# Kernel tuning notes

Measured on AMD Instinct MI355X. Metric: run time of the kernel, lower is better.

The kernel has to match this reference:

```python
import jax, jax.numpy as jnp
import numpy as np

N = 8192   # nodes per modality
D = 128    # hidden_channels
H = 2      # transformer heads
R = 15     # relations in HeteroConv (use_speaker='no')
E = 16384  # edges per relation
L = 2      # num_layers
# relation src/dst node-type ids: 0=audio, 1=text, 2=visual (dict order: a/v/t past, a/v/t future, a/v/t self, then cross)
SRC = np.array([0, 2, 1, 0, 2, 1, 0, 2, 1, 0, 0, 2, 2, 1, 1])
DST = np.array([0, 2, 1, 0, 2, 1, 0, 2, 1, 2, 1, 0, 1, 0, 2])


def setup_inputs() -> dict:
    key = jax.random.key(0)
    ks = jax.random.split(key, 18)
    f = lambda k, sh: jax.random.normal(k, sh, dtype=jnp.float32) * 0.05
    return {
        "x_audio": jax.random.normal(ks[0], (N, D), jnp.float32),
        "x_text": jax.random.normal(ks[1], (N, D), jnp.float32),
        "x_visual": jax.random.normal(ks[2], (N, D), jnp.float32),
        "edge_index": jax.random.randint(ks[3], (R, 2, E), 0, N, jnp.int32),
        "Wrel": f(ks[4], (L, R, D, D)),
        "brel": f(ks[5], (L, R, D)),
        "Wroot": f(ks[6], (L, R, D, D)),
        "Wq": f(ks[7], (D, H * D)), "bq": f(ks[8], (H * D,)),
        "Wk": f(ks[9], (D, H * D)), "bk": f(ks[10], (H * D,)),
        "Wv": f(ks[11], (D, H * D)), "bv": f(ks[12], (H * D,)),
        "Wskip": f(ks[13], (D, D)), "bskip": f(ks[14], (D,)),
        "gamma": jnp.ones((D,), jnp.float32),
        "beta": jnp.zeros((D,), jnp.float32),
    }


def reference(x_audio, x_text, x_visual, edge_index, Wrel, brel, Wroot,
              Wq, bq, Wk, bk, Wv, bv, Wskip, bskip, gamma, beta):
    src_t = jnp.asarray(SRC)
    dst_t = jnp.asarray(DST)
    x = jnp.stack([x_audio, x_text, x_visual])           # [3, N, D]
    src_idx = edge_index[:, 0]                            # [R, E]
    dst_idx = edge_index[:, 1]                            # [R, E]
    rel = jnp.arange(R)

    # --- HeteroConv of 15 GraphConvs (aggr='add' inside, 'mean' over the 5 relations per dst type) ---
    seg = (rel[:, None] * N + dst_idx).reshape(-1)        # per-relation segment ids
    for l in range(L):
        feats = jnp.take_along_axis(x[src_t], src_idx[:, :, None], axis=1)     # [R, E, D]
        msg = jax.ops.segment_sum(feats.reshape(R * E, D), seg,
                                  num_segments=R * N).reshape(R, N, D)          # scatter-add per relation
        out = (jnp.einsum('rnd,rde->rne', msg, Wrel[l]) + brel[l][:, None, :]
               + jnp.einsum('rnd,rde->rne', x[dst_t], Wroot[l]))                # lin_rel(agg) + lin_root(x_dst)
        x = jax.nn.relu(jnp.zeros_like(x).at[dst_t].add(out) / 5.0)            # mean over 5 relations per dst

    # --- hetero_to_homo: concat audio, text, visual (offsets 0, N, 2N) ---
    hx = x.reshape(3 * N, D)
    src_h = (src_t[:, None] * N + src_idx).reshape(-1)    # [R*E]
    dst_h = (dst_t[:, None] * N + dst_idx).reshape(-1)

    # --- TransformerConv (concat=False -> head mean, root skip) ---
    q = (hx @ Wq + bq).reshape(3 * N, H, D)
    k = (hx @ Wk + bk).reshape(3 * N, H, D)
    v = (hx @ Wv + bv).reshape(3 * N, H, D)
    logits = jnp.einsum('ehd,ehd->eh', q[dst_h], k[src_h]) / jnp.sqrt(jnp.float32(D))
    m = jax.ops.segment_max(logits, dst_h, num_segments=3 * N)
    p = jnp.exp(logits - m[dst_h])
    denom = jax.ops.segment_sum(p, dst_h, num_segments=3 * N)
    alpha = p / denom[dst_h]                              # segment softmax over incoming edges
    agg = jax.ops.segment_sum(alpha[:, :, None] * v[src_h], dst_h, num_segments=3 * N)  # [3N, H, D]
    out = agg.mean(axis=1) + hx @ Wskip + bskip

    # --- BatchNorm1d (training-mode batch stats) + leaky_relu ---
    mu = out.mean(axis=0)
    var = ((out - mu) ** 2).mean(axis=0)
    y = (out - mu) / jnp.sqrt(var + 1e-5) * gamma + beta
    y = jax.nn.leaky_relu(y)                              # negative_slope=0.01 (torch default)
    return y.reshape(3, N, D)                             # [audio, text, visual]
```

## Files before the change

### kernel.cpp

```cpp
#include <hip/hip_runtime.h>
#include <hip/hip_bf16.h>

#define NN 8192
#define DD 128
#define HH 2
#define RR 15
#define EE 16384
#define NLAYER 2
#define NMOD 3
#define TN (NMOD*NN)
#define NE (RR*EE)

#define SRC_BITS 0x16818618u
#define DST_BITS 0x21198618u
__device__ __forceinline__ int srcOf(int r) { return (SRC_BITS >> (2 * r)) & 3; }
__device__ __forceinline__ int dstOf(int r) { return (DST_BITS >> (2 * r)) & 3; }

typedef __attribute__((ext_vector_type(8))) short bf16x8;
typedef __attribute__((ext_vector_type(4))) float f32x4;
typedef __attribute__((ext_vector_type(4))) unsigned short u16x4;

__device__ __forceinline__ unsigned short f2bf(float v) {
    union { float f; unsigned int u; } x; x.f = v;
    unsigned int r = (x.u + 0x7fffu + ((x.u >> 16) & 1u)) >> 16;
    return (unsigned short)r;
}
__device__ __forceinline__ float bf2f(unsigned int bits16) {
    return __uint_as_float(bits16 << 16);
}
__device__ __forceinline__ float4 cvt4(u16x4 v) {
    float4 r;
    r.x = bf2f(v.x); r.y = bf2f(v.y); r.z = bf2f(v.z); r.w = bf2f(v.w);
    return r;
}

__global__ void transp_bf(const float* __restrict__ src, unsigned short* __restrict__ dst, int C) {
    int mat = blockIdx.y;
    const float* s = src + (size_t)mat * 128 * C;
    unsigned short* d = dst + (size_t)mat * 128 * C;
    for (int t = blockIdx.x * 256 + threadIdx.x; t < 128 * C; t += gridDim.x * 256) {
        int k = t / C, c = t - k * C;
        d[c * 128 + k] = f2bf(s[t]);
    }
}

__global__ void transp_qkvs(const float* __restrict__ Wq, const float* __restrict__ Wk,
                            const float* __restrict__ Wv, const float* __restrict__ Wskip,
                            unsigned short* __restrict__ WqT, unsigned short* __restrict__ WkT,
                            unsigned short* __restrict__ WvT, unsigned short* __restrict__ WskipT) {
    int y = blockIdx.y;
    const float* s = (y == 0) ? Wq : (y == 1) ? Wk : (y == 2) ? Wv : Wskip;
    unsigned short* d = (y == 0) ? WqT : (y == 1) ? WkT : (y == 2) ? WvT : WskipT;
    int C = (y == 3) ? 128 : 256;
    for (int t = blockIdx.x * 256 + threadIdx.x; t < 128 * C; t += gridDim.x * 256) {
        int k = t / C, c = t - k * C;
        d[c * 128 + k] = f2bf(s[t]);
    }
}

__global__ void wroot_prep(const float* __restrict__ Wroot, const float* __restrict__ brel,
                           unsigned short* __restrict__ WsumT, float* __restrict__ bsum) {
    int mat = blockIdx.y;
    int l = mat / 3, m = mat % 3;
    for (int t = blockIdx.x * 256 + threadIdx.x; t < 16384; t += gridDim.x * 256) {
        int k = t >> 7, c = t & 127;
        float s = 0.f;
        #pragma unroll
        for (int r = 0; r < RR; r++)
            if (((DST_BITS >> (2 * r)) & 3) == (unsigned)m) s += Wroot[(size_t)(l * RR + r) * 16384 + t];
        WsumT[(size_t)mat * 16384 + c * 128 + k] = f2bf(s);
    }
    if (blockIdx.x == 0 && threadIdx.x < 128) {
        float s = 0.f;
        #pragma unroll
        for (int r = 0; r < RR; r++)
            if (((DST_BITS >> (2 * r)) & 3) == (unsigned)m) s += brel[(l * RR + r) * 128 + threadIdx.x];
        bsum[mat * 128 + threadIdx.x] = s;
    }
}

__global__ void pack_x_bf(const float* __restrict__ xa, const float* __restrict__ xt,
                          const float* __restrict__ xv, unsigned short* __restrict__ xb) {
    int i = blockIdx.x * 256 + threadIdx.x;
    if (i < NN * DD) {
        xb[i] = f2bf(xa[i]);
        xb[NN * DD + i] = f2bf(xt[i]);
        xb[2 * NN * DD + i] = f2bf(xv[i]);
    }
}

__global__ void count_edges(const int* __restrict__ edge, int* __restrict__ cnt) {
    int t = blockIdx.x * 256 + threadIdx.x;
    if (t >= NE) return;
    int r = t >> 14, e = t & (EE - 1);
    int dst = edge[r * 2 * EE + EE + e];
    atomicAdd(&cnt[dstOf(r) * NN + dst], 1);
}

__global__ void scan_kernel(const int* __restrict__ cnt, int* __restrict__ startA,
                            int* __restrict__ cursor) {
    __shared__ int part[1024];
    int t = threadIdx.x;
    int base = t * (TN / 1024);
    int s = 0;
    for (int i = 0; i < TN / 1024; i++) s += cnt[base + i];
    part[t] = s;
    __syncthreads();
    for (int ofs = 1; ofs < 1024; ofs <<= 1) {
        int v = (t >= ofs) ? part[t - ofs] : 0;
        __syncthreads();
        part[t] += v;
        __syncthreads();
    }
    int run = (t == 0) ? 0 : part[t - 1];
    for (int i = 0; i < TN / 1024; i++) {
        startA[base + i] = run;
        cursor[base + i] = run;
        run += cnt[base + i];
    }
    if (t == 1023) startA[TN] = part[1023];
}

__global__ void place_edges(const int* __restrict__ edge, int* __restrict__ cursor,
                            unsigned int* __restrict__ sorted) {
    int t = blockIdx.x * 256 + threadIdx.x;
    if (t >= NE) return;
    int r = t >> 14, e = t & (EE - 1);
    int src = edge[r * 2 * EE + e];
    int dst = edge[r * 2 * EE + EE + e];
    int pos = atomicAdd(&cursor[dstOf(r) * NN + dst], 1);
    sorted[pos] = ((unsigned int)r << 13) | (unsigned int)src;
}

template<int MODE>
__device__ __forceinline__ void gemm_tile(const unsigned short* __restrict__ A,
                                          const unsigned short* __restrict__ BT,
                                          const float* __restrict__ bias,
                                          void* __restrict__ Cout,
                                          int ldc, int colofs, int row0,
                                          unsigned short* lds) {
    unsigned short* Alds = lds;
    unsigned short* Blds = lds + 16384;
    const int tid = threadIdx.x;
    const int lane = tid & 63;
    const int w = tid >> 6;
    #pragma unroll
    for (int i = 0; i < 8; i++) {
        int c = i * 256 + tid;
        int row = c >> 4;
        int k0 = (c & 15) << 3;
        uint4 va = *(const uint4*)(A + (size_t)(row0 + row) * 128 + k0);
        *(uint4*)((char*)Alds + (((row * 256 + k0 * 2)) ^ ((row & 7) << 4))) = va;
        uint4 vb = *(const uint4*)(BT + (size_t)row * 128 + k0);
        *(uint4*)((char*)Blds + (((row * 256 + k0 * 2)) ^ ((row & 7) << 4))) = vb;
    }
    __syncthreads();
    f32x4 acc[2][8];
    #pragma unroll
    for (int mi = 0; mi < 2; mi++)
        #pragma unroll
        for (int nj = 0; nj < 8; nj++) acc[mi][nj] = (f32x4){0.f, 0.f, 0.f, 0.f};
    const int lr = lane & 15, lk = lane >> 4;
    #pragma unroll
    for (int ks = 0; ks < 4; ks++) {
        bf16x8 a[2], b[8];
        #pragma unroll
        for (int mi = 0; mi < 2; mi++) {
            int row = w * 32 + mi * 16 + lr;
            a[mi] = *(const bf16x8*)((char*)Alds + ((row * 256 + (ks * 32 + lk * 8) * 2) ^ ((row & 7) << 4)));
        }
        #pragma unroll
        for (int nj = 0; nj < 8; nj++) {
            int row = nj * 16 + lr;
            b[nj] = *(const bf16x8*)((char*)Blds + ((row * 256 + (ks * 32 + lk * 8) * 2) ^ ((row & 7) << 4)));
        }
        #pragma unroll
        for (int mi = 0; mi < 2; mi++)
            #pragma unroll
            for (int nj = 0; nj < 8; nj++)
                acc[mi][nj] = __builtin_amdgcn_mfma_f32_16x16x32_bf16(a[mi], b[nj], acc[mi][nj], 0, 0, 0);
    }
    __syncthreads();
    float* Clds = (float*)lds;
    #pragma unroll
    for (int mi = 0; mi < 2; mi++) {
        #pragma unroll
        for (int nj = 0; nj < 8; nj++) {
            int ccl = nj * 16 + lr;
            float bb = bias ? bias[ccl] : 0.f;
            #pragma unroll
            for (int r = 0; r < 4; r++) {
                int row = w * 32 + mi * 16 + lk * 4 + r;
                Clds[row * 128 + ccl] = acc[mi][nj][r] + bb;
            }
        }
    }
    __syncthreads();
    #pragma unroll
    for (int p = 0; p < 8; p++) {
        int row = p * 16 + (tid >> 4);
        int c0 = (tid & 15) * 8;
        float4 fa = *(const float4*)(Clds + row * 128 + c0);
        float4 fb = *(const float4*)(Clds + row * 128 + c0 + 4);
        if (MODE == 2) {
            unsigned r0 = (unsigned)f2bf(fa.x) | ((unsigned)f2bf(fa.y) << 16);
            unsigned r1 = (unsigned)f2bf(fa.z) | ((unsigned)f2bf(fa.w) << 16);
            unsigned r2 = (unsigned)f2bf(fb.x) | ((unsigned)f2bf(fb.y) << 16);
            unsigned r3 = (unsigned)f2bf(fb.z) | ((unsigned)f2bf(fb.w) << 16);
            uint4 pk = {r0, r1, r2, r3};
            *(uint4*)((unsigned short*)Cout + (size_t)(row0 + row) * ldc + colofs + c0) = pk;
        } else {
            float* Cf = (float*)Cout;
            *(float4*)(Cf + (size_t)(row0 + row) * ldc + colofs + c0) = fa;
            *(float4*)(Cf + (size_t)(row0 + row) * ldc + colofs + c0 + 4) = fb;
        }
    }
}

__global__ __launch_bounds__(256) void zroot_gemm(const unsigned short* __restrict__ xbf,
                                                  const unsigned short* __restrict__ WrelT_l,
                                                  const unsigned short* __restrict__ WrootSumT_l,
                                                  const float* __restrict__ brelSum_l,
                                                  unsigned short* __restrict__ z,
                                                  float* __restrict__ xroot) {
    __shared__ unsigned short lds[2 * 16384];
    int y = blockIdx.y;
    if (y < RR) {
        gemm_tile<2>(xbf + (size_t)srcOf(y) * NN * 128, WrelT_l + (size_t)y * 16384, nullptr,
                     z + (size_t)y * NN * 128, 128, 0, blockIdx.x * 128, lds);
    } else {
        int m = y - RR;
        gemm_tile<0>(xbf + (size_t)m * NN * 128, WrootSumT_l + (size_t)m * 16384, brelSum_l + m * 128,
                     xroot + (size_t)m * NN * 128, 128, 0, blockIdx.x * 128, lds);
    }
}

__global__ __launch_bounds__(256) void qkvskip_gemm(const unsigned short* __restrict__ xbf,
                                                    const unsigned short* __restrict__ WqT,
                                                    const unsigned short* __restrict__ WkT,
                                                    const unsigned short* __restrict__ WvT,
                                                    const unsigned short* __restrict__ WskipT,
                                                    const float* __restrict__ bq,
                                                    const float* __restrict__ bk,
                                                    const float* __restrict__ bv,
                                                    const float* __restrict__ bskip,
                                                    unsigned short* __restrict__ qb,
                                                    unsigned short* __restrict__ kb,
                                                    unsigned short* __restrict__ vb,
                                                    float* __restrict__ out) {
    __shared__ unsigned short lds[2 * 16384];
    int y = blockIdx.y;
    if (y < 6) {
        int which = y >> 1, half = y & 1;
        const unsigned short* BT = (which == 0 ? WqT : which == 1 ? WkT : WvT) + half * 16384;
        const float* bias = (which == 0 ? bq : which == 1 ? bk : bv) + half * 128;
        unsigned short* C = (which == 0 ? qb : which == 1 ? kb : vb);
        gemm_tile<2>(xbf, BT, bias, C, 256, half * 128, blockIdx.x * 128, lds);
    } else {
        gemm_tile<0>(xbf, WskipT, bskip, out, 128, 0, blockIdx.x * 128, lds);
    }
}

__global__ __launch_bounds__(256) void gather_relu(const unsigned short* __restrict__ z,
                                                   const float* __restrict__ xroot,
                                                   const unsigned int* __restrict__ sorted,
                                                   const int* __restrict__ startA,
                                                   unsigned short* __restrict__ xout) {
    int node = blockIdx.x * 4 + (threadIdx.x >> 6);
    int lane = threadIdx.x & 63;
    int s = startA[node], e = startA[node + 1];
    float a0 = 0.f, a1 = 0.f, b0 = 0.f, b1 = 0.f;
    int i = s;
    for (; i + 2 <= e; i += 2) {
        unsigned int v0 = sorted[i], v1 = sorted[i + 1];
        unsigned int w0 = *(const unsigned int*)(z + ((size_t)v0 << 7) + lane * 2);
        unsigned int w1 = *(const unsigned int*)(z + ((size_t)v1 << 7) + lane * 2);
        a0 += bf2f(w0 & 0xffffu); a1 += bf2f(w0 >> 16);
        b0 += bf2f(w1 & 0xffffu); b1 += bf2f(w1 >> 16);
    }
    if (i < e) {
        unsigned int v0 = sorted[i];
        unsigned int w0 = *(const unsigned int*)(z + ((size_t)v0 << 7) + lane * 2);
        a0 += bf2f(w0 & 0xffffu); a1 += bf2f(w0 >> 16);
    }
    const float2 rt = *(const float2*)(xroot + ((size_t)node << 7) + lane * 2);
    float v0f = (rt.x + a0 + b0) * 0.2f; v0f = v0f > 0.f ? v0f : 0.f;
    float v1f = (rt.y + a1 + b1) * 0.2f; v1f = v1f > 0.f ? v1f : 0.f;
    unsigned int o = (unsigned int)f2bf(v0f) | ((unsigned int)f2bf(v1f) << 16);
    *(unsigned int*)(xout + ((size_t)node << 7) + lane * 2) = o;
}

__global__ __launch_bounds__(256) void attn_fused(const unsigned short* __restrict__ qb,
                                                  const unsigned short* __restrict__ kb,
                                                  const unsigned short* __restrict__ vb,
                                                  const unsigned int* __restrict__ sorted,
                                                  const int* __restrict__ startA,
                                                  float* __restrict__ out) {
    int node = blockIdx.x * 4 + (threadIdx.x >> 6);
    int lane = threadIdx.x & 63;
    int eh = lane >> 5;
    int l = lane & 31;
    int d4 = l * 4;
    float4 q0 = cvt4(*(const u16x4*)(qb + (size_t)node * 256 + d4));
    float4 q1 = cvt4(*(const u16x4*)(qb + (size_t)node * 256 + 128 + d4));
    float m0 = -3.0e38f, m1 = -3.0e38f, s0 = 0.f, s1 = 0.f;
    float4 a0 = {0.f, 0.f, 0.f, 0.f}, a1 = {0.f, 0.f, 0.f, 0.f};
    int st = startA[node], en = startA[node + 1];
    int idx = st + eh;
    unsigned int vcur = (idx < en) ? sorted[idx] : 0u;
    for (int base = st; base < en; base += 2) {
        unsigned int vnext = (idx + 2 < en) ? sorted[idx + 2] : 0u;
        bool valid = idx < en;
        int r = vcur >> 13;
        int srch = (int)(vcur & 8191u) + srcOf(r) * NN;
        const unsigned short* krow = kb + (size_t)srch * 256;
        const unsigned short* vrow = vb + (size_t)srch * 256;
        float4 k0 = cvt4(*(const u16x4*)(krow + d4));
        float4 k1 = cvt4(*(const u16x4*)(krow + 128 + d4));
        float4 v0 = cvt4(*(const u16x4*)(vrow + d4));
        float4 v1 = cvt4(*(const u16x4*)(vrow + 128 + d4));
        float d0 = q0.x * k0.x + q0.y * k0.y + q0.z * k0.z + q0.w * k0.w;
        float d1 = q1.x * k1.x + q1.y * k1.y + q1.z * k1.z + q1.w * k1.w;
        #pragma unroll
        for (int off = 16; off >= 1; off >>= 1) {
            d0 += __shfl_xor(d0, off);
            d1 += __shfl_xor(d1, off);
        }
        float l0 = d0 * 0.08838834764831845f;
        float l1 = d1 * 0.08838834764831845f;
        float mn0 = fmaxf(m0, l0), mn1 = fmaxf(m1, l1);
        float sc0 = __expf(m0 - mn0), sc1 = __expf(m1 - mn1);
        float p0 = valid ? __expf(l0 - mn0) : 0.f;
        float p1 = valid ? __expf(l1 - mn1) : 0.f;
        s0 = s0 * sc0 + p0;
        s1 = s1 * sc1 + p1;
        a0.x = a0.x * sc0 + p0 * v0.x; a0.y = a0.y * sc0 + p0 * v0.y;
        a0.z = a0.z * sc0 + p0 * v0.z; a0.w = a0.w * sc0 + p0 * v0.w;
        a1.x = a1.x * sc1 + p1 * v1.x; a1.y = a1.y * sc1 + p1 * v1.y;
        a1.z = a1.z * sc1 + p1 * v1.z; a1.w = a1.w * sc1 + p1 * v1.w;
        m0 = mn0; m1 = mn1;
        vcur = vnext;
        idx += 2;
    }
    float mo0 = __shfl_xor(m0, 32), so0 = __shfl_xor(s0, 32);
    float mo1 = __shfl_xor(m1, 32), so1 = __shfl_xor(s1, 32);
    float M0 = fmaxf(m0, mo0), M1 = fmaxf(m1, mo1);
    float e0 = __expf(m0 - M0), eo0 = __expf(mo0 - M0);
    float e1 = __expf(m1 - M1), eo1 = __expf(mo1 - M1);
    float S0 = s0 * e0 + so0 * eo0;
    float S1 = s1 * e1 + so1 * eo1;
    float4 A0, A1;
    A0.x = a0.x * e0 + __shfl_xor(a0.x, 32) * eo0;
    A0.y = a0.y * e0 + __shfl_xor(a0.y, 32) * eo0;
    A0.z = a0.z * e0 + __shfl_xor(a0.z, 32) * eo0;
    A0.w = a0.w * e0 + __shfl_xor(a0.w, 32) * eo0;
    A1.x = a1.x * e1 + __shfl_xor(a1.x, 32) * eo1;
    A1.y = a1.y * e1 + __shfl_xor(a1.y, 32) * eo1;
    A1.z = a1.z * e1 + __shfl_xor(a1.z, 32) * eo1;
    A1.w = a1.w * e1 + __shfl_xor(a1.w, 32) * eo1;
    if (eh == 0) {
        float inv0 = (S0 > 0.f) ? 0.5f / S0 : 0.f;
        float inv1 = (S1 > 0.f) ? 0.5f / S1 : 0.f;
        float* op = out + (size_t)node * 128 + d4;
        float4 skip4 = *(const float4*)op;
        float4 res;
        res.x = A0.x * inv0 + A1.x * inv1 + skip4.x;
        res.y = A0.y * inv0 + A1.y * inv1 + skip4.y;
        res.z = A0.z * inv0 + A1.z * inv1 + skip4.z;
        res.w = A0.w * inv0 + A1.w * inv1 + skip4.w;
        *(float4*)op = res;
    }
}

__global__ void colstats(const float* __restrict__ outb, float* __restrict__ stats) {
    int col = threadIdx.x & 127;
    int sub = threadIdx.x >> 7;
    float s = 0.f, ss = 0.f;
    for (int row = blockIdx.x * 2 + sub; row < TN; row += gridDim.x * 2) {
        float vv = outb[(size_t)row * DD + col];
        s += vv;
        ss += vv * vv;
    }
    __shared__ float red[2][256];
    red[0][threadIdx.x] = s;
    red[1][threadIdx.x] = ss;
    __syncthreads();
    if (sub == 0) {
        s  += red[0][threadIdx.x + 128];
        ss += red[1][threadIdx.x + 128];
        atomicAdd(&stats[col], s);
        atomicAdd(&stats[DD + col], ss);
    }
}

__global__ void ln_act(float* __restrict__ outb, const float* __restrict__ stats,
                       const float* __restrict__ gamma, const float* __restrict__ beta) {
    int i = blockIdx.x * 256 + threadIdx.x;
    if (i >= TN * DD) return;
    int col = i & 127;
    float mu = stats[col] * (1.f / TN);
    float var = stats[DD + col] * (1.f / TN) - mu * mu;
    float inv = rsqrtf(var + 1e-5f);
    float vv = (outb[i] - mu) * inv * gamma[col] + beta[col];
    outb[i] = vv > 0.f ? vv : 0.01f * vv;
}

extern "C" void kernel_launch(void* const* d_in, const int* in_sizes, int n_in,
                              void* d_out, int out_size, void* d_ws, size_t ws_size,
                              hipStream_t stream) {
    const float* x_audio = (const float*)d_in[0];
    const float* x_text  = (const float*)d_in[1];
    const float* x_vis   = (const float*)d_in[2];
    const int*   edge    = (const int*)d_in[3];
    const float* Wrel    = (const float*)d_in[4];
    const float* brel    = (const float*)d_in[5];
    const float* Wroot   = (const float*)d_in[6];
    const float* Wq      = (const float*)d_in[7];
    const float* bq      = (const float*)d_in[8];
    const float* Wk      = (const float*)d_in[9];
    const float* bk      = (const float*)d_in[10];
    const float* Wv      = (const float*)d_in[11];
    const float* bv      = (const float*)d_in[12];
    const float* Wskip   = (const float*)d_in[13];
    const float* bskip   = (const float*)d_in[14];
    const float* gamma   = (const float*)d_in[15];
    const float* beta    = (const float*)d_in[16];
    float* out = (float*)d_out;

    char* p = (char*)d_ws;
    unsigned short* xbfA = (unsigned short*)p; p += (size_t)TN * 128 * 2;
    unsigned short* xbfB = (unsigned short*)p; p += (size_t)TN * 128 * 2;
    unsigned short* zqkv = (unsigned short*)p; p += (size_t)3 * TN * 256 * 2;
    unsigned short* z  = zqkv;
    unsigned short* qb = zqkv;
    unsigned short* kb = zqkv + (size_t)TN * 256;
    unsigned short* vb = zqkv + (size_t)2 * TN * 256;
    float* xroot = (float*)p; p += (size_t)TN * 128 * 4;
    unsigned short* WrelT = (unsigned short*)p; p += (size_t)2 * RR * 16384 * 2;
    unsigned short* WrootSumT = (unsigned short*)p; p += (size_t)6 * 16384 * 2;
    float* brelSum = (float*)p; p += 6 * 128 * 4;
    unsigned short* WqT = (unsigned short*)p; p += 256 * 128 * 2;
    unsigned short* WkT = (unsigned short*)p; p += 256 * 128 * 2;
    unsigned short* WvT = (unsigned short*)p; p += 256 * 128 * 2;
    unsigned short* WskipT = (unsigned short*)p; p += 128 * 128 * 2;
    unsigned int* sorted = (unsigned int*)p; p += (size_t)NE * 4;
    int* startA = (int*)p; p += (TN + 1) * 4;
    int* cursor = (int*)p; p += (TN + 1) * 4;
    int* cnt = (int*)p; p += TN * 4;
    float* stats = (float*)p; p += 256 * 4;
    size_t needed = (size_t)(p - (char*)d_ws);
    if (ws_size < needed) return;

    transp_bf<<<dim3(64, 2 * RR), 256, 0, stream>>>(Wrel, WrelT, 128);
    wroot_prep<<<dim3(64, 6), 256, 0, stream>>>(Wroot, brel, WrootSumT, brelSum);
    transp_qkvs<<<dim3(64, 4), 256, 0, stream>>>(Wq, Wk, Wv, Wskip, WqT, WkT, WvT, WskipT);
    pack_x_bf<<<(NN * DD) / 256, 256, 0, stream>>>(x_audio, x_text, x_vis, xbfA);

    hipMemsetAsync(cnt, 0, (TN + 2 * DD) * 4, stream);
    count_edges<<<NE / 256, 256, 0, stream>>>(edge, cnt);
    scan_kernel<<<1, 1024, 0, stream>>>(cnt, startA, cursor);
    place_edges<<<NE / 256, 256, 0, stream>>>(edge, cursor, sorted);

    unsigned short* xcur = xbfA;
    unsigned short* xnxt = xbfB;
    for (int l = 0; l < NLAYER; ++l) {
        zroot_gemm<<<dim3(NN / 128, RR + NMOD), 256, 0, stream>>>(
            xcur, WrelT + (size_t)l * RR * 16384, WrootSumT + (size_t)l * NMOD * 16384,
            brelSum + l * NMOD * 128, z, xroot);
        gather_relu<<<TN / 4, 256, 0, stream>>>(z, xroot, sorted, startA, xnxt);
        unsigned short* t = xcur; xcur = xnxt; xnxt = t;
    }

    qkvskip_gemm<<<dim3(TN / 128, 7), 256, 0, stream>>>(xcur, WqT, WkT, WvT, WskipT,
                                                        bq, bk, bv, bskip, qb, kb, vb, out);
    attn_fused<<<TN / 4, 256, 0, stream>>>(qb, kb, vb, sorted, startA, out);

    colstats<<<96, 256, 0, stream>>>(out, stats);
    ln_act<<<(TN * DD) / 256, 256, 0, stream>>>(out, stats, gamma, beta);
}
```

Before: 243.0 us.

## Fuse prep kernels, store root term in bf16, widen gather/attention lanes to 16B loads

Merges the four weight/input preparation kernels and the counter memset into a single prep_all launch. The root-GEMM output is now stored as bf16 rather than fp32, halving its write and read traffic. gather_relu and attn_fused now have each wavefront process four edges in parallel with 16-byte loads per lane, then combine the groups with shuffles. ln_act is vectorised to float4. Together these aim to cut launch overhead and memory traffic, at the cost of extra bf16 rounding on the root term and more shuffle reductions.

```diff
diff --git a/kernel.cpp b/kernel.cpp
--- a/kernel.cpp
+++ b/kernel.cpp
@@ -18,7 +18,6 @@
 
 typedef __attribute__((ext_vector_type(8))) short bf16x8;
 typedef __attribute__((ext_vector_type(4))) float f32x4;
-typedef __attribute__((ext_vector_type(4))) unsigned short u16x4;
 
 __device__ __forceinline__ unsigned short f2bf(float v) {
     union { float f; unsigned int u; } x; x.f = v;
@@ -28,64 +27,71 @@
 __device__ __forceinline__ float bf2f(unsigned int bits16) {
     return __uint_as_float(bits16 << 16);
 }
-__device__ __forceinline__ float4 cvt4(u16x4 v) {
-    float4 r;
-    r.x = bf2f(v.x); r.y = bf2f(v.y); r.z = bf2f(v.z); r.w = bf2f(v.w);
-    return r;
-}
-
-__global__ void transp_bf(const float* __restrict__ src, unsigned short* __restrict__ dst, int C) {
-    int mat = blockIdx.y;
-    const float* s = src + (size_t)mat * 128 * C;
-    unsigned short* d = dst + (size_t)mat * 128 * C;
-    for (int t = blockIdx.x * 256 + threadIdx.x; t < 128 * C; t += gridDim.x * 256) {
-        int k = t / C, c = t - k * C;
-        d[c * 128 + k] = f2bf(s[t]);
-    }
-}
-
-__global__ void transp_qkvs(const float* __restrict__ Wq, const float* __restrict__ Wk,
-                            const float* __restrict__ Wv, const float* __restrict__ Wskip,
-                            unsigned short* __restrict__ WqT, unsigned short* __restrict__ WkT,
-                            unsigned short* __restrict__ WvT, unsigned short* __restrict__ WskipT) {
+__device__ __forceinline__ void bfu4(uint4 u, float* f) {
+    f[0] = bf2f(u.x & 0xffffu); f[1] = bf2f(u.x >> 16);
+    f[2] = bf2f(u.y & 0xffffu); f[3] = bf2f(u.y >> 16);
+    f[4] = bf2f(u.z & 0xffffu); f[5] = bf2f(u.z >> 16);
+    f[6] = bf2f(u.w & 0xffffu); f[7] = bf2f(u.w >> 16);
+}
+
+__global__ __launch_bounds__(256) void prep_all(
+        const float* __restrict__ Wrel, const float* __restrict__ Wroot,
+        const float* __restrict__ brel,
+        const float* __restrict__ Wq, const float* __restrict__ Wk,
+        const float* __restrict__ Wv, const float* __restrict__ Wskip,
+        const float* __restrict__ xa, const float* __restrict__ xt,
+        const float* __restrict__ xv,
+        unsigned short* __restrict__ WrelT, unsigned short* __restrict__ WsumT,
+        float* __restrict__ bsum,
+        unsigned short* __restrict__ WqT, unsigned short* __restrict__ WkT,
+        unsigned short* __restrict__ WvT, unsigned short* __restrict__ WskipT,
+        unsigned short* __restrict__ xb, int* __restrict__ cnt) {
     int y = blockIdx.y;
-    const float* s = (y == 0) ? Wq : (y == 1) ? Wk : (y == 2) ? Wv : Wskip;
-    unsigned short* d = (y == 0) ? WqT : (y == 1) ? WkT : (y == 2) ? WvT : WskipT;
-    int C = (y == 3) ? 128 : 256;
-    for (int t = blockIdx.x * 256 + threadIdx.x; t < 128 * C; t += gridDim.x * 256) {
-        int k = t / C, c = t - k * C;
-        d[c * 128 + k] = f2bf(s[t]);
-    }
-}
-
-__global__ void wroot_prep(const float* __restrict__ Wroot, const float* __restrict__ brel,
-                           unsigned short* __restrict__ WsumT, float* __restrict__ bsum) {
-    int mat = blockIdx.y;
-    int l = mat / 3, m = mat % 3;
-    for (int t = blockIdx.x * 256 + threadIdx.x; t < 16384; t += gridDim.x * 256) {
+    int t = blockIdx.x * 256 + threadIdx.x;
+    if (y < 30) {
+        int k = t >> 7, c = t & 127;
+        WrelT[(size_t)y * 16384 + c * 128 + k] = f2bf(Wrel[(size_t)y * 16384 + t]);
+    } else if (y < 36) {
+        int mat = y - 30, l = mat / 3, m = mat % 3;
         int k = t >> 7, c = t & 127;
         float s = 0.f;
         #pragma unroll
         for (int r = 0; r < RR; r++)
             if (((DST_BITS >> (2 * r)) & 3) == (unsigned)m) s += Wroot[(size_t)(l * RR + r) * 16384 + t];
         WsumT[(size_t)mat * 16384 + c * 128 + k] = f2bf(s);
-    }
-    if (blockIdx.x == 0 && threadIdx.x < 128) {
-        float s = 0.f;
-        #pragma unroll
-        for (int r = 0; r < RR; r++)
-            if (((DST_BITS >> (2 * r)) & 3) == (unsigned)m) s += brel[(l * RR + r) * 128 + threadIdx.x];
-        bsum[mat * 128 + threadIdx.x] = s;
-    }
-}
-
-__global__ void pack_x_bf(const float* __restrict__ xa, const float* __restrict__ xt,
-                          const float* __restrict__ xv, unsigned short* __restrict__ xb) {
-    int i = blockIdx.x * 256 + threadIdx.x;
-    if (i < NN * DD) {
-        xb[i] = f2bf(xa[i]);
-        xb[NN * DD + i] = f2bf(xt[i]);
-        xb[2 * NN * DD + i] = f2bf(xv[i]);
+        if (blockIdx.x == 0 && threadIdx.x < 128) {
+            float b = 0.f;
+            #pragma unroll
+            for (int r = 0; r < RR; r++)
+                if (((DST_BITS >> (2 * r)) & 3) == (unsigned)m) b += brel[(l * RR + r) * 128 + threadIdx.x];
+            bsum[mat * 128 + threadIdx.x] = b;
+        }
+    } else if (y < 39) {
+        int which = y - 36;
+        const float* s = which == 0 ? Wq : which == 1 ? Wk : Wv;
+        unsigned short* d = which == 0 ? WqT : which == 1 ? WkT : WvT;
+        #pragma unroll
+        for (int it = 0; it < 2; it++) {
+            int tt = t + it * 16384;
+            int k = tt >> 8, c = tt & 255;
+            d[c * 128 + k] = f2bf(s[tt]);
+        }
+    } else if (y == 39) {
+        int k = t >> 7, c = t & 127;
+        WskipT[c * 128 + k] = f2bf(Wskip[t]);
+    } else if (y == 40) {
+        for (int i = t; i < TN + 256; i += 16384) cnt[i] = 0;
+    } else {
+        int m = y - 41;
+        const float* s = m == 0 ? xa : m == 1 ? xt : xv;
+        unsigned short* d = xb + (size_t)m * NN * DD;
+        for (int i = t * 4; i < NN * DD; i += 16384 * 4) {
+            float4 v = *(const float4*)(s + i);
+            uint2 o;
+            o.x = (unsigned)f2bf(v.x) | ((unsigned)f2bf(v.y) << 16);
+            o.y = (unsigned)f2bf(v.z) | ((unsigned)f2bf(v.w) << 16);
+            *(uint2*)(d + i) = o;
+        }
     }
 }
 
@@ -222,7 +228,7 @@
                                                   const unsigned short* __restrict__ WrootSumT_l,
                                                   const float* __restrict__ brelSum_l,
                                                   unsigned short* __restrict__ z,
-                                                  float* __restrict__ xroot) {
+                                                  unsigned short* __restrict__ xroot) {
     __shared__ unsigned short lds[2 * 16384];
     int y = blockIdx.y;
     if (y < RR) {
@@ -230,7 +236,7 @@
                      z + (size_t)y * NN * 128, 128, 0, blockIdx.x * 128, lds);
     } else {
         int m = y - RR;
-        gemm_tile<0>(xbf + (size_t)m * NN * 128, WrootSumT_l + (size_t)m * 16384, brelSum_l + m * 128,
+        gemm_tile<2>(xbf + (size_t)m * NN * 128, WrootSumT_l + (size_t)m * 16384, brelSum_l + m * 128,
                      xroot + (size_t)m * NN * 128, 128, 0, blockIdx.x * 128, lds);
     }
 }
@@ -262,32 +268,51 @@
 }
 
 __global__ __launch_bounds__(256) void gather_relu(const unsigned short* __restrict__ z,
-                                                   const float* __restrict__ xroot,
+                                                   const unsigned short* __restrict__ xroot,
                                                    const unsigned int* __restrict__ sorted,
                                                    const int* __restrict__ startA,
                                                    unsigned short* __restrict__ xout) {
     int node = blockIdx.x * 4 + (threadIdx.x >> 6);
     int lane = threadIdx.x & 63;
-    int s = startA[node], e = startA[node + 1];
-    float a0 = 0.f, a1 = 0.f, b0 = 0.f, b1 = 0.f;
-    int i = s;
-    for (; i + 2 <= e; i += 2) {
-        unsigned int v0 = sorted[i], v1 = sorted[i + 1];
-        unsigned int w0 = *(const unsigned int*)(z + ((size_t)v0 << 7) + lane * 2);
-        unsigned int w1 = *(const unsigned int*)(z + ((size_t)v1 << 7) + lane * 2);
-        a0 += bf2f(w0 & 0xffffu); a1 += bf2f(w0 >> 16);
-        b0 += bf2f(w1 & 0xffffu); b1 += bf2f(w1 >> 16);
-    }
-    if (i < e) {
-        unsigned int v0 = sorted[i];
-        unsigned int w0 = *(const unsigned int*)(z + ((size_t)v0 << 7) + lane * 2);
-        a0 += bf2f(w0 & 0xffffu); a1 += bf2f(w0 >> 16);
-    }
-    const float2 rt = *(const float2*)(xroot + ((size_t)node << 7) + lane * 2);
-    float v0f = (rt.x + a0 + b0) * 0.2f; v0f = v0f > 0.f ? v0f : 0.f;
-    float v1f = (rt.y + a1 + b1) * 0.2f; v1f = v1f > 0.f ? v1f : 0.f;
-    unsigned int o = (unsigned int)f2bf(v0f) | ((unsigned int)f2bf(v1f) << 16);
-    *(unsigned int*)(xout + ((size_t)node << 7) + lane * 2) = o;
+    int g = lane >> 4, p = lane & 15;
+    int st = startA[node], en = startA[node + 1];
+    float acc[8];
+    #pragma unroll
+    for (int j = 0; j < 8; j++) acc[j] = 0.f;
+    int idx = st + g;
+    unsigned int vcur = (idx < en) ? sorted[idx] : 0u;
+    for (int base = st; base < en; base += 4) {
+        unsigned int vnext = (idx + 4 < en) ? sorted[idx + 4] : 0u;
+        uint4 u = *(const uint4*)(z + ((size_t)vcur << 7) + p * 8);
+        if (idx < en) {
+            float f[8]; bfu4(u, f);
+            #pragma unroll
+            for (int j = 0; j < 8; j++) acc[j] += f[j];
+        }
+        vcur = vnext;
+        idx += 4;
+    }
+    #pragma unroll
+    for (int j = 0; j < 8; j++) {
+        acc[j] += __shfl_xor(acc[j], 32);
+        acc[j] += __shfl_xor(acc[j], 16);
+    }
+    if (g == 0) {
+        uint4 rt = *(const uint4*)(xroot + ((size_t)node << 7) + p * 8);
+        float r[8]; bfu4(rt, r);
+        unsigned short o[8];
+        #pragma unroll
+        for (int j = 0; j < 8; j++) {
+            float v = (r[j] + acc[j]) * 0.2f;
+            o[j] = f2bf(v > 0.f ? v : 0.f);
+        }
+        uint4 pk;
+        pk.x = (unsigned)o[0] | ((unsigned)o[1] << 16);
+        pk.y = (unsigned)o[2] | ((unsigned)o[3] << 16);
+        pk.z = (unsigned)o[4] | ((unsigned)o[5] << 16);
+        pk.w = (unsigned)o[6] | ((unsigned)o[7] << 16);
+        *(uint4*)(xout + ((size_t)node << 7) + p * 8) = pk;
+    }
 }
 
 __global__ __launch_bounds__(256) void attn_fused(const unsigned short* __restrict__ qb,
@@ -298,31 +323,35 @@
                                                   float* __restrict__ out) {
     int node = blockIdx.x * 4 + (threadIdx.x >> 6);
     int lane = threadIdx.x & 63;
-    int eh = lane >> 5;
-    int l = lane & 31;
-    int d4 = l * 4;
-    float4 q0 = cvt4(*(const u16x4*)(qb + (size_t)node * 256 + d4));
-    float4 q1 = cvt4(*(const u16x4*)(qb + (size_t)node * 256 + 128 + d4));
+    int g = lane >> 4, p = lane & 15;
+    float q0[8], q1[8];
+    bfu4(*(const uint4*)(qb + (size_t)node * 256 + p * 8), q0);
+    bfu4(*(const uint4*)(qb + (size_t)node * 256 + 128 + p * 8), q1);
     float m0 = -3.0e38f, m1 = -3.0e38f, s0 = 0.f, s1 = 0.f;
-    float4 a0 = {0.f, 0.f, 0.f, 0.f}, a1 = {0.f, 0.f, 0.f, 0.f};
+    float a0[8], a1[8];
+    #pragma unroll
+    for (int j = 0; j < 8; j++) { a0[j] = 0.f; a1[j] = 0.f; }
     int st = startA[node], en = startA[node + 1];
-    int idx = st + eh;
+    int idx = st + g;
     unsigned int vcur = (idx < en) ? sorted[idx] : 0u;
-    for (int base = st; base < en; base += 2) {
-        unsigned int vnext = (idx + 2 < en) ? sorted[idx + 2] : 0u;
+    for (int base = st; base < en; base += 4) {
+        unsigned int vnext = (idx + 4 < en) ? sorted[idx + 4] : 0u;
         bool valid = idx < en;
         int r = vcur >> 13;
         int srch = (int)(vcur & 8191u) + srcOf(r) * NN;
         const unsigned short* krow = kb + (size_t)srch * 256;
         const unsigned short* vrow = vb + (size_t)srch * 256;
-        float4 k0 = cvt4(*(const u16x4*)(krow + d4));
-        float4 k1 = cvt4(*(const u16x4*)(krow + 128 + d4));
-        float4 v0 = cvt4(*(const u16x4*)(vrow + d4));
-        float4 v1 = cvt4(*(const u16x4*)(vrow + 128 + d4));
-        float d0 = q0.x * k0.x + q0.y * k0.y + q0.z * k0.z + q0.w * k0.w;
-        float d1 = q1.x * k1.x + q1.y * k1.y + q1.z * k1.z + q1.w * k1.w;
-        #pragma unroll
-        for (int off = 16; off >= 1; off >>= 1) {
+        uint4 k0r = *(const uint4*)(krow + p * 8);
+        uint4 k1r = *(const uint4*)(krow + 128 + p * 8);
+        uint4 v0r = *(const uint4*)(vrow + p * 8);
+        uint4 v1r = *(const uint4*)(vrow + 128 + p * 8);
+        float k0[8], k1[8];
+        bfu4(k0r, k0); bfu4(k1r, k1);
+        float d0 = 0.f, d1 = 0.f;
+        #pragma unroll
+        for (int j = 0; j < 8; j++) { d0 += q0[j] * k0[j]; d1 += q1[j] * k1[j]; }
+        #pragma unroll
+        for (int off = 8; off >= 1; off >>= 1) {
             d0 += __shfl_xor(d0, off);
             d1 += __shfl_xor(d1, off);
         }
@@ -334,41 +363,50 @@
         float p1 = valid ? __expf(l1 - mn1) : 0.f;
         s0 = s0 * sc0 + p0;
         s1 = s1 * sc1 + p1;
-        a0.x = a0.x * sc0 + p0 * v0.x; a0.y = a0.y * sc0 + p0 * v0.y;
-        a0.z = a0.z * sc0 + p0 * v0.z; a0.w = a0.w * sc0 + p0 * v0.w;
-        a1.x = a1.x * sc1 + p1 * v1.x; a1.y = a1.y * sc1 + p1 * v1.y;
-        a1.z = a1.z * sc1 + p1 * v1.z; a1.w = a1.w * sc1 + p1 * v1.w;
+        float v0[8], v1[8];
+        bfu4(v0r, v0); bfu4(v1r, v1);
+        #pragma unroll
+        for (int j = 0; j < 8; j++) {
+            a0[j] = a0[j] * sc0 + p0 * v0[j];
+            a1[j] = a1[j] * sc1 + p1 * v1[j];
+        }
         m0 = mn0; m1 = mn1;
         vcur = vnext;
-        idx += 2;
-    }
-    float mo0 = __shfl_xor(m0, 32), so0 = __shfl_xor(s0, 32);
-    float mo1 = __shfl_xor(m1, 32), so1 = __shfl_xor(s1, 32);
-    float M0 = fmaxf(m0, mo0), M1 = fmaxf(m1, mo1);
-    float e0 = __expf(m0 - M0), eo0 = __expf(mo0 - M0);
-    float e1 = __expf(m1 - M1), eo1 = __expf(mo1 - M1);
-    float S0 = s0 * e0 + so0 * eo0;
-    float S1 = s1 * e1 + so1 * eo1;
-    float4 A0, A1;
-    A0.x = a0.x * e0 + __shfl_xor(a0.x, 32) * eo0;
-    A0.y = a0.y * e0 + __shfl_xor(a0.y, 32) * eo0;
-    A0.z = a0.z * e0 + __shfl_xor(a0.z, 32) * eo0;
-    A0.w = a0.w * e0 + __shfl_xor(a0.w, 32) * eo0;
-    A1.x = a1.x * e1 + __shfl_xor(a1.x, 32) * eo1;
-    A1.y = a1.y * e1 + __shfl_xor(a1.y, 32) * eo1;
-    A1.z = a1.z * e1 + __shfl_xor(a1.z, 32) * eo1;
-    A1.w = a1.w * e1 + __shfl_xor(a1.w, 32) * eo1;
-    if (eh == 0) {
-        float inv0 = (S0 > 0.f) ? 0.5f / S0 : 0.f;
-        float inv1 = (S1 > 0.f) ? 0.5f / S1 : 0.f;
-        float* op = out + (size_t)node * 128 + d4;
-        float4 skip4 = *(const float4*)op;
-        float4 res;
-        res.x = A0.x * inv0 + A1.x * inv1 + skip4.x;
-        res.y = A0.y * inv0 + A1.y * inv1 + skip4.y;
-        res.z = A0.z * inv0 + A1.z * inv1 + skip4.z;
-        res.w = A0.w * inv0 + A1.w * inv1 + skip4.w;
-        *(float4*)op = res;
+        idx += 4;
+    }
+    #pragma unroll
+    for (int off = 32; off >= 16; off >>= 1) {
+        float mo0 = __shfl_xor(m0, off), so0 = __shfl_xor(s0, off);
+        float mo1 = __shfl_xor(m1, off), so1 = __shfl_xor(s1, off);
+        float M0 = fmaxf(m0, mo0), M1 = fmaxf(m1, mo1);
+        float e0 = __expf(m0 - M0), eo0 = __expf(mo0 - M0);
+        float e1 = __expf(m1 - M1), eo1 = __expf(mo1 - M1);
+        s0 = s0 * e0 + so0 * eo0;
+        s1 = s1 * e1 + so1 * eo1;
+        #pragma unroll
+        for (int j = 0; j < 8; j++) {
+            a0[j] = a0[j] * e0 + __shfl_xor(a0[j], off) * eo0;
+            a1[j] = a1[j] * e1 + __shfl_xor(a1[j], off) * eo1;
+        }
+        m0 = M0; m1 = M1;
+    }
+    if (g == 0) {
+        float inv0 = (s0 > 0.f) ? 0.5f / s0 : 0.f;
+        float inv1 = (s1 > 0.f) ? 0.5f / s1 : 0.f;
+        float* op = out + (size_t)node * 128 + p * 8;
+        float4 ska = *(const float4*)op;
+        float4 skb = *(const float4*)(op + 4);
+        float4 ra, rb;
+        ra.x = a0[0] * inv0 + a1[0] * inv1 + ska.x;
+        ra.y = a0[1] * inv0 + a1[1] * inv1 + ska.y;
+        ra.z = a0[2] * inv0 + a1[2] * inv1 + ska.z;
+        ra.w = a0[3] * inv0 + a1[3] * inv1 + ska.w;
+        rb.x = a0[4] * inv0 + a1[4] * inv1 + skb.x;
+        rb.y = a0[5] * inv0 + a1[5] * inv1 + skb.y;
+        rb.z = a0[6] * inv0 + a1[6] * inv1 + skb.z;
+        rb.w = a0[7] * inv0 + a1[7] * inv1 + skb.w;
+        *(float4*)op = ra;
+        *(float4*)(op + 4) = rb;
     }
 }
 
@@ -395,14 +433,22 @@
 
 __global__ void ln_act(float* __restrict__ outb, const float* __restrict__ stats,
                        const float* __restrict__ gamma, const float* __restrict__ beta) {
-    int i = blockIdx.x * 256 + threadIdx.x;
+    int i = (blockIdx.x * 256 + threadIdx.x) * 4;
     if (i >= TN * DD) return;
     int col = i & 127;
-    float mu = stats[col] * (1.f / TN);
-    float var = stats[DD + col] * (1.f / TN) - mu * mu;
-    float inv = rsqrtf(var + 1e-5f);
-    float vv = (outb[i] - mu) * inv * gamma[col] + beta[col];
-    outb[i] = vv > 0.f ? vv : 0.01f * vv;
+    float4 v = *(const float4*)(outb + i);
+    float o[4] = {v.x, v.y, v.z, v.w};
+    #pragma unroll
+    for (int j = 0; j < 4; j++) {
+        int c = col + j;
+        float mu = stats[c] * (1.f / TN);
+        float var = stats[DD + c] * (1.f / TN) - mu * mu;
+        float inv = rsqrtf(var + 1e-5f);
+        float vv = (o[j] - mu) * inv * gamma[c] + beta[c];
+        o[j] = vv > 0.f ? vv : 0.01f * vv;
+    }
+    float4 res = {o[0], o[1], o[2], o[3]};
+    *(float4*)(outb + i) = res;
 }
 
 extern "C" void kernel_launch(void* const* d_in, const int* in_sizes, int n_in,
@@ -435,7 +481,7 @@
     unsigned short* qb = zqkv;
     unsigned short* kb = zqkv + (size_t)TN * 256;
     unsigned short* vb = zqkv + (size_t)2 * TN * 256;
-    float* xroot = (float*)p; p += (size_t)TN * 128 * 4;
+    unsigned short* xroot = (unsigned short*)p; p += (size_t)TN * 128 * 2;
     unsigned short* WrelT = (unsigned short*)p; p += (size_t)2 * RR * 16384 * 2;
     unsigned short* WrootSumT = (unsigned short*)p; p += (size_t)6 * 16384 * 2;
     float* brelSum = (float*)p; p += 6 * 128 * 4;
@@ -451,12 +497,11 @@
     size_t needed = (size_t)(p - (char*)d_ws);
     if (ws_size < needed) return;
 
-    transp_bf<<<dim3(64, 2 * RR), 256, 0, stream>>>(Wrel, WrelT, 128);
-    wroot_prep<<<dim3(64, 6), 256, 0, stream>>>(Wroot, brel, WrootSumT, brelSum);
-    transp_qkvs<<<dim3(64, 4), 256, 0, stream>>>(Wq, Wk, Wv, Wskip, WqT, WkT, WvT, WskipT);
-    pack_x_bf<<<(NN * DD) / 256, 256, 0, stream>>>(x_audio, x_text, x_vis, xbfA);
-
-    hipMemsetAsync(cnt, 0, (TN + 2 * DD) * 4, stream);
+    prep_all<<<dim3(64, 44), 256, 0, stream>>>(Wrel, Wroot, brel, Wq, Wk, Wv, Wskip,
+                                               x_audio, x_text, x_vis,
+                                               WrelT, WrootSumT, brelSum,
+                                               WqT, WkT, WvT, WskipT, xbfA, cnt);
+
     count_edges<<<NE / 256, 256, 0, stream>>>(edge, cnt);
     scan_kernel<<<1, 1024, 0, stream>>>(cnt, startA, cursor);
     place_edges<<<NE / 256, 256, 0, stream>>>(edge, cursor, sorted);
@@ -476,5 +521,5 @@
     attn_fused<<<TN / 4, 256, 0, stream>>>(qb, kb, vb, sorted, startA, out);
 
     colstats<<<96, 256, 0, stream>>>(out, stats);
-    ln_act<<<(TN * DD) / 256, 256, 0, stream>>>(out, stats, gamma, beta);
-}
+    ln_act<<<(TN * DD) / 1024, 256, 0, stream>>>(out, stats, gamma, beta);
+}
```

Measured after the change: 222.6 us. 1.09x faster.
